# Optimization experiments

Measured on AMD Instinct MI355X. Metric: run time of the kernel, lower is better.

Reference implementation:

```python
import jax, jax.numpy as jnp
import numpy as np

B, T, D = 64, 512, 1024   # batch, seq, input_dim
R, O = 1024, 1024          # recurrent_dim, output_dim


def setup_inputs() -> dict:
    key = jax.random.key(0)
    ks = jax.random.split(key, 8)
    s_in = 1.0 / np.sqrt(D)
    s_rec = 1.0 / np.sqrt(R)
    return {
        "x": jax.random.normal(ks[0], (B, T, D), dtype=jnp.float32),
        "Wxh": jax.random.uniform(ks[1], (R, D), jnp.float32, -s_in, s_in),
        "bh": jax.random.uniform(ks[2], (R,), jnp.float32, -s_in, s_in),
        "Whh": jax.random.uniform(ks[3], (R, R), jnp.float32, -s_rec, s_rec),
        "Wxz": jax.random.uniform(ks[4], (R, D), jnp.float32, -s_in, s_in),
        "bz": jax.random.uniform(ks[5], (R,), jnp.float32, -s_in, s_in),
        "Whz": jax.random.uniform(ks[6], (R, R), jnp.float32, -s_rec, s_rec),
        "Wy": jax.random.uniform(ks[7], (O, R), jnp.float32, -s_rec, s_rec),
        "by": jnp.zeros((O,), dtype=jnp.float32),
    }


def reference(x, Wxh, bh, Whh, Wxz, bz, Whz, Wy, by):
    # Original per-step math (note the quirk: h2z output is added to x_t
    # BEFORE x2z):
    #   z  = sigmoid(Wxz @ (x_t + Whz @ h) + bz)
    #   hb = relu(Wxh @ x_t + bh + Whh @ h)
    #   h  = z * h + (1 - z) * hb
    # Precompute all input-side GEMMs in one batched contraction (linearity);
    # fold Wxz@Whz into a single recurrent matrix.
    xh = jnp.einsum('btd,rd->btr', x, Wxh) + bh          # [B,T,R]
    xz = jnp.einsum('btd,rd->btr', x, Wxz) + bz          # [B,T,R]
    Mz = Wxz @ Whz                                        # [R,R]

    def step(h, inp):
        xh_t, xz_t = inp                                  # each [B,R]
        z = jax.nn.sigmoid(xz_t + h @ Mz.T)
        hb = jax.nn.relu(xh_t + h @ Whh.T)
        h = z * h + (1.0 - z) * hb
        return h, None

    h0 = jnp.zeros((x.shape[0], Whh.shape[0]), dtype=x.dtype)
    # scan over time: move T to leading axis
    h_final, _ = jax.lax.scan(
        step, h0, (jnp.swapaxes(xh, 0, 1), jnp.swapaxes(xz, 0, 1)))
    return h_final @ Wy.T + by                            # [B,O]
```

## Files before the change

kernel.cpp:

```cpp
#include <hip/hip_runtime.h>

#define BB 64
#define TT 512
#define DD 1024
#define RR 1024

#define SCAN_BLOCKS 32
#define HS_STRIDE 1032
#define SCAN_LDS_BYTES (64 * HS_STRIDE * 2)

typedef __bf16 bf16x8 __attribute__((ext_vector_type(8)));
typedef float f32x4 __attribute__((ext_vector_type(4)));
typedef unsigned short us4 __attribute__((ext_vector_type(4)));
typedef unsigned int u32x4 __attribute__((ext_vector_type(4)));
typedef unsigned long long u64;

__device__ inline unsigned short f2bf(float f) {
  unsigned int u = __float_as_uint(f);
  u = (u + 0x7fffu + ((u >> 16) & 1u)) >> 16;
  return (unsigned short)u;
}
__device__ inline float bf2f(unsigned short b) {
  return __uint_as_float(((unsigned int)b) << 16);
}

__device__ inline u32x4 ld16_sc(const void* p) {
  u32x4 r;
  asm volatile("global_load_dwordx4 %0, %1, off sc0 sc1"
               : "=v"(r) : "v"(p) : "memory");
  return r;
}

__global__ void k_f2b4(const float* __restrict__ in, unsigned short* __restrict__ out, int n4) {
  int i = blockIdx.x * blockDim.x + threadIdx.x;
  if (i < n4) {
    const float4 v = ((const float4*)in)[i];
    us4 o;
    o.x = f2bf(v.x); o.y = f2bf(v.y); o.z = f2bf(v.z); o.w = f2bf(v.w);
    ((us4*)out)[i] = o;
  }
}

__global__ __launch_bounds__(256) void k_transpose_bf16(
    const float* __restrict__ in, unsigned short* __restrict__ out) {
  __shared__ float tile[32][33];
  const int bx = blockIdx.x * 32, by0 = blockIdx.y * 32;
  const int tx = threadIdx.x, ty = threadIdx.y;
#pragma unroll
  for (int r = 0; r < 32; r += 8)
    tile[ty + r][tx] = in[(size_t)(by0 + ty + r) * 1024 + bx + tx];
  __syncthreads();
#pragma unroll
  for (int r = 0; r < 32; r += 8)
    out[(size_t)(bx + ty + r) * 1024 + by0 + tx] = f2bf(tile[tx][ty + r]);
}

__device__ inline void gload_lds16(const unsigned short* g, unsigned short* l) {
  __builtin_amdgcn_global_load_lds(
      (const __attribute__((address_space(1))) unsigned int*)g,
      (__attribute__((address_space(3))) unsigned int*)l, 16, 0, 0);
}

template <int EPI>
__global__ __launch_bounds__(256) void gemm_bt(
    const unsigned short* __restrict__ A,
    const unsigned short* __restrict__ Bm,
    const float* __restrict__ bias_h,
    const float* __restrict__ bias_z,
    unsigned short* __restrict__ outb, int K) {
  __shared__ __attribute__((aligned(16))) unsigned short As[128 * 32];
  __shared__ __attribute__((aligned(16))) unsigned short Bs[128 * 32];
  const int tid = threadIdx.x;
  const int m0 = blockIdx.y * 128, n0 = blockIdx.x * 128;
  const int lane = tid & 63, wid = tid >> 6;
  const int l16 = lane & 15, quad = lane >> 4;
  const int wm = (wid & 1) * 64, wn = (wid >> 1) * 64;

  f32x4 acc[4][4] = {};

  const int c0 = tid, c1 = 256 + tid;
  const int rowA0 = c0 >> 2, colA0 = (c0 & 3) << 3;
  const int rowA1 = c1 >> 2, colA1 = (c1 & 3) << 3;

  for (int kk = 0; kk < K; kk += 32) {
    __syncthreads();
    gload_lds16(A + (size_t)(m0 + rowA0) * K + kk + colA0, As + c0 * 8);
    gload_lds16(A + (size_t)(m0 + rowA1) * K + kk + colA1, As + c1 * 8);
    gload_lds16(Bm + (size_t)(n0 + rowA0) * K + kk + colA0, Bs + c0 * 8);
    gload_lds16(Bm + (size_t)(n0 + rowA1) * K + kk + colA1, Bs + c1 * 8);
    __syncthreads();
    bf16x8 af[4], bfr[4];
#pragma unroll
    for (int i = 0; i < 4; ++i) {
      af[i] = *(const bf16x8*)&As[(wm + i * 16 + l16) * 32 + quad * 8];
      bfr[i] = *(const bf16x8*)&Bs[(wn + i * 16 + l16) * 32 + quad * 8];
    }
#pragma unroll
    for (int i = 0; i < 4; ++i)
#pragma unroll
      for (int j = 0; j < 4; ++j)
        acc[i][j] = __builtin_amdgcn_mfma_f32_16x16x32_bf16(af[i], bfr[j], acc[i][j], 0, 0, 0);
  }

#pragma unroll
  for (int i = 0; i < 4; ++i) {
#pragma unroll
    for (int j = 0; j < 4; ++j) {
#pragma unroll
      for (int r = 0; r < 4; ++r) {
        const int m = m0 + wm + i * 16 + quad * 4 + r;
        const int n = n0 + wn + j * 16 + l16;
        float v = acc[i][j][r];
        if (EPI == 0) {
          v += (n < 1024) ? bias_h[n] : bias_z[n - 1024];
          const int b = m >> 9;
          const int t = m & 511;
          outb[((size_t)(t * 64 + b) << 11) + n] = f2bf(v);
        } else {
          outb[(size_t)m * 1024 + n] = f2bf(v);
        }
      }
    }
  }
}

__global__ __launch_bounds__(1024) void scan_out_k(
    const unsigned short* __restrict__ xhz,
    const unsigned short* __restrict__ Wrec,
    const unsigned short* __restrict__ Wyb,
    const float* __restrict__ by,
    unsigned short* __restrict__ hb0, unsigned short* __restrict__ hb1,
    unsigned int* __restrict__ flags,
    float* __restrict__ out) {
  extern __shared__ char smem[];
  unsigned short* hs = (unsigned short*)smem;
  float* red = (float*)smem;

  const int tid = threadIdx.x, g = blockIdx.x;
  const int lane = tid & 63, wid = tid >> 6;
  const int l16 = lane & 15, quad = lane >> 4;
  const int ks = wid >> 2, nsub = wid & 3;
  const int kw = ks * 256;
  const int i0 = g * 32;

  const int bcol = (nsub < 2) ? (i0 + nsub * 16 + l16)
                              : (1024 + i0 + (nsub - 2) * 16 + l16);
  const unsigned short* Bb = Wrec + (size_t)bcol * 1024 + kw + quad * 8;
  bf16x8 bfr[8];
#pragma unroll
  for (int s = 0; s < 8; ++s) bfr[s] = *(const bf16x8*)(Bb + s * 32);

  const int sr = tid >> 4;
  const int su = tid & 15;
  const unsigned short* gsrc_base0 = hb0 + sr * 1024 + su * 8;
  const unsigned short* gsrc_base1 = hb1 + sr * 1024 + su * 8;
  unsigned short* ldst = hs + sr * HS_STRIDE + su * 8;

  const int eb = tid >> 4, ej = (tid & 15) * 2;
  float hold0 = 0.0f, hold1 = 0.0f;

  const unsigned short* hbc = hb0;
  unsigned short* hbn = hb1;
  const unsigned short* gsrc = gsrc_base0;

  for (int tt = 0; tt < TT; ++tt) {
    u32x4 tmp[8];
#pragma unroll
    for (int c = 0; c < 8; ++c)
      tmp[c] = ld16_sc((const char*)gsrc + c * 256);
    const size_t xrow = ((size_t)(tt * 64 + eb)) << 11;
    const unsigned int xh2 = *(const unsigned int*)(xhz + xrow + i0 + ej);
    const unsigned int xz2 = *(const unsigned int*)(xhz + xrow + 1024 + i0 + ej);
    asm volatile("s_waitcnt vmcnt(0)" ::: "memory");
#pragma unroll
    for (int c = 0; c < 8; ++c)
      *(u32x4*)(ldst + c * 128) = tmp[c];
    __syncthreads();

    f32x4 acc[4] = {};
#pragma unroll
    for (int s = 0; s < 8; ++s) {
#pragma unroll
      for (int mt = 0; mt < 4; ++mt) {
        const bf16x8 afr = *(const bf16x8*)(hs + (mt * 16 + l16) * HS_STRIDE + kw + s * 32 + quad * 8);
        acc[mt] = __builtin_amdgcn_mfma_f32_16x16x32_bf16(afr, bfr[s], acc[mt], 0, 0, 0);
      }
    }
    __syncthreads();

#pragma unroll
    for (int mt = 0; mt < 4; ++mt)
#pragma unroll
      for (int r = 0; r < 4; ++r)
        red[(size_t)(ks * 64 + mt * 16 + quad * 4 + r) * 68 + nsub * 16 + l16] = acc[mt][r];
    __syncthreads();

    float ph0 = 0.f, ph1 = 0.f, pz0 = 0.f, pz1 = 0.f;
#pragma unroll
    for (int w = 0; w < 4; ++w) {
      const float* rb = red + (size_t)(w * 64 + eb) * 68;
      ph0 += rb[ej]; ph1 += rb[ej + 1];
      pz0 += rb[32 + ej]; pz1 += rb[32 + ej + 1];
    }
    {
      const float xh0 = bf2f((unsigned short)(xh2 & 0xffff));
      const float xh1 = bf2f((unsigned short)(xh2 >> 16));
      const float xz0 = bf2f((unsigned short)(xz2 & 0xffff));
      const float xz1 = bf2f((unsigned short)(xz2 >> 16));
      const float z0 = 1.0f / (1.0f + __expf(-(xz0 + pz0)));
      const float z1 = 1.0f / (1.0f + __expf(-(xz1 + pz1)));
      const float hb_0 = fmaxf(xh0 + ph0, 0.0f);
      const float hb_1 = fmaxf(xh1 + ph1, 0.0f);
      hold0 = z0 * hold0 + (1.0f - z0) * hb_0;
      hold1 = z1 * hold1 + (1.0f - z1) * hb_1;
      const unsigned int pk = (unsigned int)f2bf(hold0) | ((unsigned int)f2bf(hold1) << 16);
      __hip_atomic_store((unsigned int*)(hbn + eb * 1024 + i0 + ej), pk,
                         __ATOMIC_RELAXED, __HIP_MEMORY_SCOPE_AGENT);
    }

    __syncthreads();
    if (tid == 0)
      __hip_atomic_store(&flags[g], (unsigned int)(tt + 1),
                         __ATOMIC_RELAXED, __HIP_MEMORY_SCOPE_AGENT);
    if (tid < 64) {
      const unsigned int tgt = (unsigned int)(tt + 1);
      unsigned int v;
      do {
        v = __hip_atomic_load(&flags[tid & 31], __ATOMIC_RELAXED, __HIP_MEMORY_SCOPE_AGENT);
      } while (__any(v < tgt));
    }
    __syncthreads();

    const unsigned short* tc = hbc; hbc = hbn; hbn = (unsigned short*)tc;
    gsrc = (tt & 1) ? gsrc_base0 : gsrc_base1;
  }

  {
    u32x4 tmp[8];
#pragma unroll
    for (int c = 0; c < 8; ++c)
      tmp[c] = ld16_sc((const char*)(hbc + sr * 1024 + su * 8) + c * 256);
    asm volatile("s_waitcnt vmcnt(0)" ::: "memory");
#pragma unroll
    for (int c = 0; c < 8; ++c)
      *(u32x4*)(ldst + c * 128) = tmp[c];
  }
  __syncthreads();

  if (nsub < 2) {
    const int ocol = i0 + nsub * 16 + l16;
    const unsigned short* Byb = Wyb + (size_t)ocol * 1024 + kw + quad * 8;
    f32x4 acc[4] = {};
#pragma unroll
    for (int s = 0; s < 8; ++s) {
      const bf16x8 byf = *(const bf16x8*)(Byb + s * 32);
#pragma unroll
      for (int mt = 0; mt < 4; ++mt) {
        const bf16x8 afr = *(const bf16x8*)(hs + (mt * 16 + l16) * HS_STRIDE + kw + s * 32 + quad * 8);
        acc[mt] = __builtin_amdgcn_mfma_f32_16x16x32_bf16(afr, byf, acc[mt], 0, 0, 0);
      }
    }
    __syncthreads();
#pragma unroll
    for (int mt = 0; mt < 4; ++mt)
#pragma unroll
      for (int r = 0; r < 4; ++r)
        red[(size_t)(ks * 64 + mt * 16 + quad * 4 + r) * 68 + nsub * 16 + l16] = acc[mt][r];
  } else {
    __syncthreads();
  }
  __syncthreads();

  {
    float o0 = by[i0 + ej], o1 = by[i0 + ej + 1];
#pragma unroll
    for (int w = 0; w < 4; ++w) {
      const float* rb = red + (size_t)(w * 64 + eb) * 68;
      o0 += rb[ej]; o1 += rb[ej + 1];
    }
    float2 ov; ov.x = o0; ov.y = o1;
    *(float2*)(out + (size_t)eb * 1024 + i0 + ej) = ov;
  }
}

extern "C" void kernel_launch(void* const* d_in, const int* in_sizes, int n_in,
                              void* d_out, int out_size, void* d_ws, size_t ws_size,
                              hipStream_t stream) {
  const float* x = (const float*)d_in[0];
  const float* Wxh = (const float*)d_in[1];
  const float* bh = (const float*)d_in[2];
  const float* Whh = (const float*)d_in[3];
  const float* Wxz = (const float*)d_in[4];
  const float* bz = (const float*)d_in[5];
  const float* Whz = (const float*)d_in[6];
  const float* Wy = (const float*)d_in[7];
  const float* by = (const float*)d_in[8];
  float* out = (float*)d_out;

  char* ws = (char*)d_ws;
  size_t off = 0;
  auto alloc = [&](size_t bytes) -> void* {
    void* p = ws + off;
    off += (bytes + 255) & ~(size_t)255;
    return p;
  };
  const size_t nX = (size_t)BB * TT * DD;
  unsigned short* xb = (unsigned short*)alloc(nX * 2);
  unsigned short* Wcat = (unsigned short*)alloc((size_t)2048 * 1024 * 2);
  unsigned short* WhzT = (unsigned short*)alloc((size_t)1024 * 1024 * 2);
  unsigned short* Wrec = (unsigned short*)alloc((size_t)2048 * 1024 * 2);
  unsigned short* Wyb = (unsigned short*)alloc((size_t)1024 * 1024 * 2);
  unsigned short* xhz = (unsigned short*)alloc((size_t)TT * BB * 2048 * 2);
  unsigned short* hb0 = (unsigned short*)alloc((size_t)BB * RR * 2);
  unsigned short* hb1 = (unsigned short*)alloc((size_t)BB * RR * 2);
  unsigned int* flags = (unsigned int*)alloc(1024);

  hipMemsetAsync(hb0, 0, (size_t)BB * RR * 2, stream);
  hipMemsetAsync(flags, 0, 1024, stream);

  k_f2b4<<<dim3((unsigned)(nX / 4 / 256)), 256, 0, stream>>>(x, xb, (int)(nX / 4));
  k_f2b4<<<dim3(1024), 256, 0, stream>>>(Wxh, Wcat, 262144);
  k_f2b4<<<dim3(1024), 256, 0, stream>>>(Wxz, Wcat + 1024 * 1024, 262144);
  k_f2b4<<<dim3(1024), 256, 0, stream>>>(Whh, Wrec, 262144);
  k_f2b4<<<dim3(1024), 256, 0, stream>>>(Wy, Wyb, 262144);
  k_transpose_bf16<<<dim3(32, 32), dim3(32, 8), 0, stream>>>(Whz, WhzT);

  gemm_bt<1><<<dim3(8, 8), 256, 0, stream>>>(Wcat + 1024 * 1024, WhzT, nullptr, nullptr,
                                             Wrec + (size_t)1024 * 1024, 1024);
  gemm_bt<0><<<dim3(16, 256), 256, 0, stream>>>(xb, Wcat, bh, bz, xhz, 1024);

  hipFuncSetAttribute((const void*)scan_out_k,
                      hipFuncAttributeMaxDynamicSharedMemorySize, SCAN_LDS_BYTES);
  const unsigned short* xhz_c = xhz;
  const unsigned short* Wrec_c = Wrec;
  const unsigned short* Wyb_c = Wyb;
  const float* by_c = by;
  void* kargs[] = {(void*)&xhz_c, (void*)&Wrec_c, (void*)&Wyb_c, (void*)&by_c,
                   (void*)&hb0, (void*)&hb1, (void*)&flags, (void*)&out};
  hipLaunchCooperativeKernel((void*)scan_out_k, dim3(SCAN_BLOCKS), dim3(1024),
                             kargs, SCAN_LDS_BYTES, stream);
}
```

Measured before the change: 3.379 ms.

## Split recurrent scan across 64 blocks with 16 hidden units each

Measured after the change: 3.427 ms. Within noise of the previous version (+1.4%).

```diff
diff --git a/kernel.cpp b/kernel.cpp
--- a/kernel.cpp
+++ b/kernel.cpp
@@ -5,15 +5,15 @@
 #define DD 1024
 #define RR 1024
 
-#define SCAN_BLOCKS 32
+#define SCAN_BLOCKS 64
 #define HS_STRIDE 1032
 #define SCAN_LDS_BYTES (64 * HS_STRIDE * 2)
+#define RED_STRIDE 36
 
 typedef __bf16 bf16x8 __attribute__((ext_vector_type(8)));
 typedef float f32x4 __attribute__((ext_vector_type(4)));
 typedef unsigned short us4 __attribute__((ext_vector_type(4)));
 typedef unsigned int u32x4 __attribute__((ext_vector_type(4)));
-typedef unsigned long long u64;
 
 __device__ inline unsigned short f2bf(float f) {
   unsigned int u = __float_as_uint(f);
@@ -139,12 +139,11 @@
   const int tid = threadIdx.x, g = blockIdx.x;
   const int lane = tid & 63, wid = tid >> 6;
   const int l16 = lane & 15, quad = lane >> 4;
-  const int ks = wid >> 2, nsub = wid & 3;
+  const int ks = wid >> 2, msub = (wid >> 1) & 1, nsub = wid & 1;
   const int kw = ks * 256;
-  const int i0 = g * 32;
-
-  const int bcol = (nsub < 2) ? (i0 + nsub * 16 + l16)
-                              : (1024 + i0 + (nsub - 2) * 16 + l16);
+  const int i0h = g * 16;
+
+  const int bcol = (nsub == 0) ? (i0h + l16) : (1024 + i0h + l16);
   const unsigned short* Bb = Wrec + (size_t)bcol * 1024 + kw + quad * 8;
   bf16x8 bfr[8];
 #pragma unroll
@@ -156,65 +155,59 @@
   const unsigned short* gsrc_base1 = hb1 + sr * 1024 + su * 8;
   unsigned short* ldst = hs + sr * HS_STRIDE + su * 8;
 
-  const int eb = tid >> 4, ej = (tid & 15) * 2;
-  float hold0 = 0.0f, hold1 = 0.0f;
-
-  const unsigned short* hbc = hb0;
-  unsigned short* hbn = hb1;
+  const int eb = tid >> 4, ec = tid & 15;
+  float hold = 0.0f;
+
   const unsigned short* gsrc = gsrc_base0;
 
   for (int tt = 0; tt < TT; ++tt) {
+    unsigned short* hbn = (tt & 1) ? hb0 : hb1;
+
     u32x4 tmp[8];
 #pragma unroll
     for (int c = 0; c < 8; ++c)
       tmp[c] = ld16_sc((const char*)gsrc + c * 256);
     const size_t xrow = ((size_t)(tt * 64 + eb)) << 11;
-    const unsigned int xh2 = *(const unsigned int*)(xhz + xrow + i0 + ej);
-    const unsigned int xz2 = *(const unsigned int*)(xhz + xrow + 1024 + i0 + ej);
+    const unsigned short xh = xhz[xrow + i0h + ec];
+    const unsigned short xz = xhz[xrow + 1024 + i0h + ec];
     asm volatile("s_waitcnt vmcnt(0)" ::: "memory");
 #pragma unroll
     for (int c = 0; c < 8; ++c)
       *(u32x4*)(ldst + c * 128) = tmp[c];
     __syncthreads();
 
-    f32x4 acc[4] = {};
+    f32x4 acc[2] = {};
 #pragma unroll
     for (int s = 0; s < 8; ++s) {
 #pragma unroll
-      for (int mt = 0; mt < 4; ++mt) {
-        const bf16x8 afr = *(const bf16x8*)(hs + (mt * 16 + l16) * HS_STRIDE + kw + s * 32 + quad * 8);
+      for (int mt = 0; mt < 2; ++mt) {
+        const bf16x8 afr = *(const bf16x8*)(
+            hs + (msub * 32 + mt * 16 + l16) * HS_STRIDE + kw + s * 32 + quad * 8);
         acc[mt] = __builtin_amdgcn_mfma_f32_16x16x32_bf16(afr, bfr[s], acc[mt], 0, 0, 0);
       }
     }
     __syncthreads();
 
 #pragma unroll
-    for (int mt = 0; mt < 4; ++mt)
+    for (int mt = 0; mt < 2; ++mt)
 #pragma unroll
       for (int r = 0; r < 4; ++r)
-        red[(size_t)(ks * 64 + mt * 16 + quad * 4 + r) * 68 + nsub * 16 + l16] = acc[mt][r];
-    __syncthreads();
-
-    float ph0 = 0.f, ph1 = 0.f, pz0 = 0.f, pz1 = 0.f;
+        red[(size_t)(ks * 64 + msub * 32 + mt * 16 + quad * 4 + r) * RED_STRIDE +
+            nsub * 16 + l16] = acc[mt][r];
+    __syncthreads();
+
+    float ph = 0.f, pz = 0.f;
 #pragma unroll
     for (int w = 0; w < 4; ++w) {
-      const float* rb = red + (size_t)(w * 64 + eb) * 68;
-      ph0 += rb[ej]; ph1 += rb[ej + 1];
-      pz0 += rb[32 + ej]; pz1 += rb[32 + ej + 1];
+      const float* rb = red + (size_t)(w * 64 + eb) * RED_STRIDE;
+      ph += rb[ec];
+      pz += rb[16 + ec];
     }
     {
-      const float xh0 = bf2f((unsigned short)(xh2 & 0xffff));
-      const float xh1 = bf2f((unsigned short)(xh2 >> 16));
-      const float xz0 = bf2f((unsigned short)(xz2 & 0xffff));
-      const float xz1 = bf2f((unsigned short)(xz2 >> 16));
-      const float z0 = 1.0f / (1.0f + __expf(-(xz0 + pz0)));
-      const float z1 = 1.0f / (1.0f + __expf(-(xz1 + pz1)));
-      const float hb_0 = fmaxf(xh0 + ph0, 0.0f);
-      const float hb_1 = fmaxf(xh1 + ph1, 0.0f);
-      hold0 = z0 * hold0 + (1.0f - z0) * hb_0;
-      hold1 = z1 * hold1 + (1.0f - z1) * hb_1;
-      const unsigned int pk = (unsigned int)f2bf(hold0) | ((unsigned int)f2bf(hold1) << 16);
-      __hip_atomic_store((unsigned int*)(hbn + eb * 1024 + i0 + ej), pk,
+      const float z = 1.0f / (1.0f + __expf(-(bf2f(xz) + pz)));
+      const float hbv = fmaxf(bf2f(xh) + ph, 0.0f);
+      hold = z * hold + (1.0f - z) * hbv;
+      __hip_atomic_store(hbn + (size_t)eb * 1024 + i0h + ec, f2bf(hold),
                          __ATOMIC_RELAXED, __HIP_MEMORY_SCOPE_AGENT);
     }
 
@@ -226,12 +219,11 @@
       const unsigned int tgt = (unsigned int)(tt + 1);
       unsigned int v;
       do {
-        v = __hip_atomic_load(&flags[tid & 31], __ATOMIC_RELAXED, __HIP_MEMORY_SCOPE_AGENT);
+        v = __hip_atomic_load(&flags[tid & 63], __ATOMIC_RELAXED, __HIP_MEMORY_SCOPE_AGENT);
       } while (__any(v < tgt));
     }
     __syncthreads();
 
-    const unsigned short* tc = hbc; hbc = hbn; hbn = (unsigned short*)tc;
     gsrc = (tt & 1) ? gsrc_base0 : gsrc_base1;
   }
 
@@ -239,7 +231,7 @@
     u32x4 tmp[8];
 #pragma unroll
     for (int c = 0; c < 8; ++c)
-      tmp[c] = ld16_sc((const char*)(hbc + sr * 1024 + su * 8) + c * 256);
+      tmp[c] = ld16_sc((const char*)(hb0 + sr * 1024 + su * 8) + c * 256);
     asm volatile("s_waitcnt vmcnt(0)" ::: "memory");
 #pragma unroll
     for (int c = 0; c < 8; ++c)
@@ -247,39 +239,38 @@
   }
   __syncthreads();
 
-  if (nsub < 2) {
-    const int ocol = i0 + nsub * 16 + l16;
+  f32x4 oacc[2] = {};
+  if (nsub == 0) {
+    const int ocol = i0h + l16;
     const unsigned short* Byb = Wyb + (size_t)ocol * 1024 + kw + quad * 8;
-    f32x4 acc[4] = {};
 #pragma unroll
     for (int s = 0; s < 8; ++s) {
       const bf16x8 byf = *(const bf16x8*)(Byb + s * 32);
 #pragma unroll
-      for (int mt = 0; mt < 4; ++mt) {
-        const bf16x8 afr = *(const bf16x8*)(hs + (mt * 16 + l16) * HS_STRIDE + kw + s * 32 + quad * 8);
-        acc[mt] = __builtin_amdgcn_mfma_f32_16x16x32_bf16(afr, byf, acc[mt], 0, 0, 0);
+      for (int mt = 0; mt < 2; ++mt) {
+        const bf16x8 afr = *(const bf16x8*)(
+            hs + (msub * 32 + mt * 16 + l16) * HS_STRIDE + kw + s * 32 + quad * 8);
+        oacc[mt] = __builtin_amdgcn_mfma_f32_16x16x32_bf16(afr, byf, oacc[mt], 0, 0, 0);
       }
     }
-    __syncthreads();
-#pragma unroll
-    for (int mt = 0; mt < 4; ++mt)
+  }
+  __syncthreads();
+  if (nsub == 0) {
+#pragma unroll
+    for (int mt = 0; mt < 2; ++mt)
 #pragma unroll
       for (int r = 0; r < 4; ++r)
-        red[(size_t)(ks * 64 + mt * 16 + quad * 4 + r) * 68 + nsub * 16 + l16] = acc[mt][r];
-  } else {
-    __syncthreads();
+        red[(size_t)(ks * 64 + msub * 32 + mt * 16 + quad * 4 + r) * RED_STRIDE +
+            l16] = oacc[mt][r];
   }
   __syncthreads();
 
   {
-    float o0 = by[i0 + ej], o1 = by[i0 + ej + 1];
-#pragma unroll
-    for (int w = 0; w < 4; ++w) {
-      const float* rb = red + (size_t)(w * 64 + eb) * 68;
-      o0 += rb[ej]; o1 += rb[ej + 1];
-    }
-    float2 ov; ov.x = o0; ov.y = o1;
-    *(float2*)(out + (size_t)eb * 1024 + i0 + ej) = ov;
+    float o = by[i0h + ec];
+#pragma unroll
+    for (int w = 0; w < 4; ++w)
+      o += red[(size_t)(w * 64 + eb) * RED_STRIDE + ec];
+    out[(size_t)eb * 1024 + i0h + ec] = o;
   }
 }
 
```
